# Kernel optimization log

Measured on AMD Instinct MI355X. Metric: run time of the kernel, lower is better.

## Reference

```python
import jax, jax.numpy as jnp
import numpy as np

K = 32          # neighbors per point
EPS = 1e-5      # InstanceNorm eps (torch default)
SLOPE = 0.2     # LeakyReLU negative slope


def _knn(x, k):
    # x: [B, N, C]; squared euclidean distances (same ordering as torch.cdist p=2)
    sq = jnp.sum(x * x, axis=-1)                       # [B, N]
    d = sq[:, :, None] + sq[:, None, :] - 2.0 * jnp.einsum('bnc,bmc->bnm', x, x)
    _, idx = jax.lax.top_k(-d, k + 1)                  # smallest distances first
    return idx[:, :, 1:]                               # drop self -> [B, N, k]


def _edge_feat(x, idx):
    # x: [B, N, C], idx: [B, N, k] -> [B, N, k, 2C] = concat(neighbor - center, center)
    nb = jax.vmap(lambda xb, ib: xb[ib])(x, idx)       # [B, N, k, C] gather
    c = jnp.broadcast_to(x[:, :, None, :], nb.shape)
    return jnp.concatenate([nb - c, c], axis=-1)


def _inorm(x, axes):
    # InstanceNorm (no affine): normalize over `axes` with biased variance
    m = jnp.mean(x, axis=axes, keepdims=True)
    v = jnp.mean((x - m) ** 2, axis=axes, keepdims=True)
    return (x - m) * jax.lax.rsqrt(v + EPS)


def _lrelu(x):
    return jnp.where(x >= 0, x, SLOPE * x)


def setup_inputs() -> dict:
    key = jax.random.key(0)
    ks = jax.random.split(key, 11)
    B, N = 2, 2048

    def w(k, shape):
        return jax.random.normal(k, shape, jnp.float32) * 0.05

    return {
        'x': jax.random.normal(ks[0], (B, N, 3), jnp.float32),
        'n': jax.random.normal(ks[1], (B, N, 3), jnp.float32),
        'W0': w(ks[2], (32, 6)),      # Conv2d(6, 32, 1, bias=False)
        'W1': w(ks[3], (64, 64)),     # Conv2d(64, 64, 1)
        'W2': w(ks[4], (128, 128)),   # Conv2d(128, 128, 1)
        'W3': w(ks[5], (256, 256)),   # Conv2d(256, 256, 1)
        'Wh': w(ks[6], (128, 480)),   # Conv1d(sum(hidden)=480, encod_dim=128, 1)
        'fc1_w': w(ks[7], (128, 128)),
        'fc1_b': w(ks[8], (128,)),
        'fc2_w': w(ks[9], (128, 128)),
        'fc2_b': w(ks[10], (128,)),
    }


def reference(x, n, W0, W1, W2, W3, Wh, fc1_w, fc1_b, fc2_w, fc2_b):
    # include_normals=False: n is accepted but unused (matches torch forward).
    feats = []
    h = x  # [B, N, C], C starts at 3
    for W in (W0, W1, W2, W3):
        idx = _knn(h, K)                              # [B, N, K]
        e = _edge_feat(h, idx)                        # [B, N, K, 2C]
        e = jnp.einsum('bnkc,oc->bnko', e, W)         # 1x1 conv
        e = _lrelu(_inorm(e, (1, 2)))                 # InstanceNorm2d over (N, K)
        h = jnp.max(e, axis=2)                        # max over neighbors -> [B, N, O]
        feats.append(h)
    f = jnp.concatenate(feats, axis=-1)               # [B, N, 480]
    f = jnp.einsum('bnc,oc->bno', f, Wh)              # 1x1 conv1d -> [B, N, 128]
    f = _lrelu(_inorm(f, (1,)))                       # InstanceNorm1d over N; dropout is identity (eval)
    g = jnp.max(f, axis=1)                            # adaptive_max_pool1d(1) -> [B, 128]
    g = g @ fc1_w.T + fc1_b
    # torch InstanceNorm1d on a 2D [B, 128] input treats it as unbatched (C, L):
    # normalizes each row over its 128 features.
    g = _lrelu(_inorm(g, (1,)))
    return g @ fc2_w.T + fc2_b                        # [B, 128]
```

## Files before the change

kernel.cpp:

```cpp
#include <hip/hip_runtime.h>
#include <hip/hip_bf16.h>
#include <cstdint>

using bf16 = __hip_bfloat16;

static constexpr int B = 2;
static constexpr int N = 2048;
static constexpr int KNN = 32;
static constexpr int FD = 480;
static constexpr float EPS = 1e-5f;
static constexpr float SLOPE = 0.2f;
static constexpr int REP = 8;

static constexpr size_t N_XF = (size_t)B * N * 3;
static constexpr size_t N_FEATS = (size_t)B * N * FD;
static constexpr size_t N_DIST = (size_t)B * N * N;
static constexpr size_t N_IDX = (size_t)B * N * KNN;
static constexpr size_t N_PROJ = (size_t)B * N * 512;
static constexpr size_t O_XF = 0;
static constexpr size_t O_FEATS = O_XF + N_XF;
static constexpr size_t O_DIST = O_FEATS + N_FEATS;
static constexpr size_t O_IDX = O_DIST + N_DIST;
static constexpr size_t O_PROJ = O_IDX + N_IDX;
static constexpr size_t O_WP0 = O_PROJ + N_PROJ;
static constexpr size_t O_WP1 = O_WP0 + 192;
static constexpr size_t O_WP2 = O_WP1 + 4096;
static constexpr size_t O_WP3 = O_WP2 + 16384;
static constexpr size_t O_WHT = O_WP3 + 65536;
static constexpr size_t O_F1W = O_WHT + 61440;
static constexpr size_t O_F1B = O_F1W + 16384;
static constexpr size_t O_F2W = O_F1B + 128;
static constexpr size_t O_F2B = O_F2W + 16384;
static constexpr size_t O_FLAG = O_F2B + 128;
static constexpr size_t O_CS0 = O_FLAG + 16;
static constexpr size_t O_CS1 = O_CS0 + (size_t)REP * B * 32 * 2;
static constexpr size_t O_CS2 = O_CS1 + (size_t)REP * B * 64 * 2;
static constexpr size_t O_CS3 = O_CS2 + (size_t)REP * B * 128 * 2;
static constexpr size_t O_FSUM = O_CS3 + (size_t)REP * B * 256 * 2;
static constexpr size_t O_FSS = O_FSUM + 256;
static constexpr size_t O_FMAX = O_FSS + 256;
static constexpr size_t O_END = O_FMAX + 256;
static constexpr size_t N_ZERO = O_END - O_CS0;

__device__ __forceinline__ float lrelu(float x) { return x >= 0.f ? x : SLOPE * x; }

__device__ __forceinline__ float load_in(const void* p, int i, int isf32) {
  return isf32 ? ((const float*)p)[i] : __bfloat162float(((const bf16*)p)[i]);
}

__device__ __forceinline__ unsigned key_of(float f) {
  unsigned u = __float_as_uint(f);
  return (u & 0x80000000u) ? ~u : (u | 0x80000000u);
}

static constexpr int PREP_TOTAL =
    (int)(N_XF + 96 + 2048 + 8192 + 32768 + 61440 + 16384 + 128 + 16384 + 128 + N_ZERO);

__global__ __launch_bounds__(256) void prep_kernel(
    const void* __restrict__ x, const void* __restrict__ W0, const void* __restrict__ W1,
    const void* __restrict__ W2, const void* __restrict__ W3, const void* __restrict__ Wh,
    const void* __restrict__ fc1w, const void* __restrict__ fc1b,
    const void* __restrict__ fc2w, const void* __restrict__ fc2b, float* __restrict__ ws) {
  __shared__ float red[256];
  const unsigned short* xr = (const unsigned short*)x;
  float mx = 0.f;
  for (int i = threadIdx.x; i < B * N * 3; i += 256) {
    float v = __uint_as_float(((unsigned)xr[i]) << 16);
    v = fabsf(v);
    if (!(v < 1e30f)) v = 1e30f;
    mx = fmaxf(mx, v);
  }
  red[threadIdx.x] = mx;
  __syncthreads();
  for (int s = 128; s > 0; s >>= 1) {
    if (threadIdx.x < s) red[threadIdx.x] = fmaxf(red[threadIdx.x], red[threadIdx.x + s]);
    __syncthreads();
  }
  int isf = red[0] > 1e3f ? 1 : 0;
  if (blockIdx.x == 0 && threadIdx.x == 0) ((int*)(ws + O_FLAG))[0] = isf;

  int idx = blockIdx.x * 256 + threadIdx.x;
  if (idx < (int)N_XF) { ws[O_XF + idx] = load_in(x, idx, isf); return; }
  idx -= (int)N_XF;
  if (idx < 96) {
    int o = idx / 3, c = idx - o * 3;
    float a = load_in(W0, o * 6 + c, isf);
    float bb = load_in(W0, o * 6 + 3 + c, isf);
    ws[O_WP0 + c * 64 + o] = a;
    ws[O_WP0 + c * 64 + 32 + o] = bb - a;
    return;
  }
  idx -= 96;
  if (idx < 2048) {
    int o = idx >> 5, c = idx & 31;
    float a = load_in(W1, o * 64 + c, isf);
    float bb = load_in(W1, o * 64 + 32 + c, isf);
    ws[O_WP1 + c * 128 + o] = a;
    ws[O_WP1 + c * 128 + 64 + o] = bb - a;
    return;
  }
  idx -= 2048;
  if (idx < 8192) {
    int o = idx >> 6, c = idx & 63;
    float a = load_in(W2, o * 128 + c, isf);
    float bb = load_in(W2, o * 128 + 64 + c, isf);
    ws[O_WP2 + c * 256 + o] = a;
    ws[O_WP2 + c * 256 + 128 + o] = bb - a;
    return;
  }
  idx -= 8192;
  if (idx < 32768) {
    int o = idx >> 7, c = idx & 127;
    float a = load_in(W3, o * 256 + c, isf);
    float bb = load_in(W3, o * 256 + 128 + c, isf);
    ws[O_WP3 + c * 512 + o] = a;
    ws[O_WP3 + c * 512 + 256 + o] = bb - a;
    return;
  }
  idx -= 32768;
  if (idx < 61440) {
    int o = idx / 480, c = idx - o * 480;
    ws[O_WHT + c * 128 + o] = load_in(Wh, idx, isf);
    return;
  }
  idx -= 61440;
  if (idx < 16384) { ws[O_F1W + idx] = load_in(fc1w, idx, isf); return; }
  idx -= 16384;
  if (idx < 128) { ws[O_F1B + idx] = load_in(fc1b, idx, isf); return; }
  idx -= 128;
  if (idx < 16384) { ws[O_F2W + idx] = load_in(fc2w, idx, isf); return; }
  idx -= 16384;
  if (idx < 128) { ws[O_F2B + idx] = load_in(fc2b, idx, isf); return; }
  idx -= 128;
  if (idx < (int)N_ZERO) ws[O_CS0 + idx] = 0.f;
}

template <int C>
__global__ __launch_bounds__(256) void dist_kernel(const float* __restrict__ h, int hstride,
                                                   unsigned* __restrict__ dist) {
  constexpr int CW = 16;
  __shared__ float Ast[CW][68];
  __shared__ float Bst[CW][132];
  __shared__ float sqn[64], sqm[128];
  int b = blockIdx.z;
  int n0 = blockIdx.y * 64, m0 = blockIdx.x * 128;
  int tid = threadIdx.x;
  int tx = tid & 15, ty = tid >> 4;
  float dot[4][8] = {};
  float sqa = 0.f;
  for (int cc = 0; cc < C; cc += CW) {
    if constexpr (C % CW == 0) {
      int r = tid >> 2, cq = (tid & 3) * 4;
      float4 va = *reinterpret_cast<const float4*>(
          &h[(size_t)(b * N + n0 + r) * hstride + cc + cq]);
      Ast[cq + 0][r] = va.x;
      Ast[cq + 1][r] = va.y;
      Ast[cq + 2][r] = va.z;
      Ast[cq + 3][r] = va.w;
#pragma unroll
      for (int k = 0; k < 2; ++k) {
        int i = tid + k * 256;
        int rB = i >> 2, cqB = (i & 3) * 4;
        float4 vb = *reinterpret_cast<const float4*>(
            &h[(size_t)(b * N + m0 + rB) * hstride + cc + cqB]);
        Bst[cqB + 0][rB] = vb.x;
        Bst[cqB + 1][rB] = vb.y;
        Bst[cqB + 2][rB] = vb.z;
        Bst[cqB + 3][rB] = vb.w;
      }
    } else {
      for (int i = tid; i < 64 * CW; i += 256) {
        int c = i & 15, r = i >> 4;
        int gc = cc + c;
        Ast[c][r] = (gc < C) ? h[(size_t)(b * N + n0 + r) * hstride + gc] : 0.f;
      }
      for (int i = tid; i < 128 * CW; i += 256) {
        int c = i & 15, r = i >> 4;
        int gc = cc + c;
        Bst[c][r] = (gc < C) ? h[(size_t)(b * N + m0 + r) * hstride + gc] : 0.f;
      }
    }
    __syncthreads();
    if (tid < 64) {
#pragma unroll
      for (int c = 0; c < CW; ++c) { float v = Ast[c][tid]; sqa += v * v; }
    } else if (tid < 192) {
      int r = tid - 64;
#pragma unroll
      for (int c = 0; c < CW; ++c) { float v = Bst[c][r]; sqa += v * v; }
    }
#pragma unroll
    for (int c = 0; c < CW; ++c) {
      float4 a0 = *reinterpret_cast<const float4*>(&Ast[c][ty * 4]);
      float4 b0 = *reinterpret_cast<const float4*>(&Bst[c][tx * 4]);
      float4 b1 = *reinterpret_cast<const float4*>(&Bst[c][64 + tx * 4]);
      float av[4] = {a0.x, a0.y, a0.z, a0.w};
      float bv[8] = {b0.x, b0.y, b0.z, b0.w, b1.x, b1.y, b1.z, b1.w};
#pragma unroll
      for (int i = 0; i < 4; ++i)
#pragma unroll
        for (int j = 0; j < 8; ++j) dot[i][j] += av[i] * bv[j];
    }
    __syncthreads();
  }
  if (tid < 64) sqn[tid] = sqa;
  else if (tid < 192) sqm[tid - 64] = sqa;
  __syncthreads();
#pragma unroll
  for (int i = 0; i < 4; ++i) {
    int nn = n0 + ty * 4 + i;
    float sn = sqn[ty * 4 + i];
    uint4 w;
    w.x = key_of(sn + sqm[tx * 4 + 0] - 2.f * dot[i][0]);
    w.y = key_of(sn + sqm[tx * 4 + 1] - 2.f * dot[i][1]);
    w.z = key_of(sn + sqm[tx * 4 + 2] - 2.f * dot[i][2]);
    w.w = key_of(sn + sqm[tx * 4 + 3] - 2.f * dot[i][3]);
    *reinterpret_cast<uint4*>(&dist[(size_t)(b * N + nn) * N + m0 + tx * 4]) = w;
    uint4 w2;
    w2.x = key_of(sn + sqm[64 + tx * 4 + 0] - 2.f * dot[i][4]);
    w2.y = key_of(sn + sqm[64 + tx * 4 + 1] - 2.f * dot[i][5]);
    w2.z = key_of(sn + sqm[64 + tx * 4 + 2] - 2.f * dot[i][6]);
    w2.w = key_of(sn + sqm[64 + tx * 4 + 3] - 2.f * dot[i][7]);
    *reinterpret_cast<uint4*>(&dist[(size_t)(b * N + nn) * N + m0 + 64 + tx * 4]) = w2;
  }
}

__device__ __forceinline__ unsigned long long wave_min_u64(unsigned long long v) {
#pragma unroll
  for (int m = 1; m < 64; m <<= 1) {
    unsigned lo = (unsigned)v;
    unsigned hi = (unsigned)(v >> 32);
    unsigned olo = (unsigned)__shfl_xor((int)lo, m, 64);
    unsigned ohi = (unsigned)__shfl_xor((int)hi, m, 64);
    unsigned long long ov = ((unsigned long long)ohi << 32) | olo;
    if (ov < v) v = ov;
  }
  return v;
}

#define ARGMIN32(dk, ld, lj)                                        \
  {                                                                 \
    unsigned kv0 = dk[0], kv1 = dk[8], kv2 = dk[16], kv3 = dk[24];  \
    int j0 = 0, j1 = 8, j2 = 16, j3 = 24;                           \
    _Pragma("unroll")                                               \
    for (int t = 1; t < 8; ++t) {                                   \
      if (dk[t] < kv0) { kv0 = dk[t]; j0 = t; }                     \
      if (dk[8 + t] < kv1) { kv1 = dk[8 + t]; j1 = 8 + t; }         \
      if (dk[16 + t] < kv2) { kv2 = dk[16 + t]; j2 = 16 + t; }      \
      if (dk[24 + t] < kv3) { kv3 = dk[24 + t]; j3 = 24 + t; }      \
    }                                                               \
    if (kv1 < kv0) { kv0 = kv1; j0 = j1; }                          \
    if (kv3 < kv2) { kv2 = kv3; j2 = j3; }                          \
    if (kv2 < kv0) { kv0 = kv2; j0 = j2; }                          \
    ld = kv0; lj = j0;                                              \
  }

__device__ __forceinline__ unsigned bitonic64_u32(unsigned v, int lane) {
#pragma unroll
  for (int k = 2; k <= 64; k <<= 1) {
#pragma unroll
    for (int j = k >> 1; j > 0; j >>= 1) {
      unsigned o = (unsigned)__shfl_xor((int)v, j, 64);
      bool up = (lane & k) == 0;
      bool lower = (lane & j) == 0;
      bool keepmin = (up == lower);
      unsigned mn = v < o ? v : o;
      unsigned mx = v < o ? o : v;
      v = keepmin ? mn : mx;
    }
  }
  return v;
}

__device__ __forceinline__ void bitonic64_u64(unsigned& hi, unsigned& lo, int lane) {
#pragma unroll
  for (int k = 2; k <= 64; k <<= 1) {
#pragma unroll
    for (int j = k >> 1; j > 0; j >>= 1) {
      unsigned ohi = (unsigned)__shfl_xor((int)hi, j, 64);
      unsigned olo = (unsigned)__shfl_xor((int)lo, j, 64);
      bool up = (lane & k) == 0;
      bool lower = (lane & j) == 0;
      bool keepmin = (up == lower);
      bool lt = (hi < ohi) || (hi == ohi && lo < olo);
      bool take_other = keepmin ? !lt : lt;
      if (take_other) { hi = ohi; lo = olo; }
    }
  }
}

template <int C, int NO2>
__global__ __launch_bounds__(256) void selproj_kernel(const unsigned* __restrict__ dist,
                                                      int* __restrict__ idxb,
                                                      const float* __restrict__ h,
                                                      int hstride,
                                                      const float* __restrict__ Wp,
                                                      float* __restrict__ projb) {
  constexpr int NSEL = B * N / 4;
  constexpr int MT = NO2 / 64;
  constexpr int CW = 16;
  __shared__ float As[64][17];
  __shared__ float Bs[64][17];
  if (blockIdx.x < NSEL) {
    int row = blockIdx.x * 4 + (threadIdx.x >> 6);
    int lane = threadIdx.x & 63;
    const unsigned* drow = dist + (size_t)row * N;
    unsigned dk[32];
#pragma unroll
    for (int j = 0; j < 32; ++j) dk[j] = drow[j * 64 + lane];
    unsigned lmin0 = dk[0], lmin1 = dk[1];
#pragma unroll
    for (int j = 2; j < 32; j += 2) {
      lmin0 = lmin0 < dk[j] ? lmin0 : dk[j];
      lmin1 = lmin1 < dk[j + 1] ? lmin1 : dk[j + 1];
    }
    unsigned lmin = lmin0 < lmin1 ? lmin0 : lmin1;
    unsigned srt = bitonic64_u32(lmin, lane);
    unsigned T = (unsigned)__shfl((int)srt, 32, 64);
    unsigned cnt = 0;
#pragma unroll
    for (int j = 0; j < 32; ++j) cnt += (dk[j] <= T) ? 1u : 0u;
    unsigned inc = cnt;
#pragma unroll
    for (int d = 1; d < 64; d <<= 1) {
      unsigned t = (unsigned)__shfl_up((int)inc, d, 64);
      if (lane >= d) inc += t;
    }
    unsigned tot = (unsigned)__shfl((int)inc, 63, 64);
    unsigned off = inc - cnt;
    bool fast = tot <= 64u;
    unsigned* aHi = reinterpret_cast<unsigned*>(&As[0][0]);
    unsigned* aLo = reinterpret_cast<unsigned*>(&Bs[0][0]);
    int wbase = (threadIdx.x >> 6) * 64;
    aHi[wbase + lane] = 0xFFFFFFFFu;
    aLo[wbase + lane] = 0xFFFFFFFFu;
    __syncthreads();
    if (fast) {
      unsigned o = off;
#pragma unroll
      for (int j = 0; j < 32; ++j) {
        if (dk[j] <= T) {
          aHi[wbase + o] = dk[j];
          aLo[wbase + o] = (unsigned)(j * 64 + lane);
          ++o;
        }
      }
    }
    __syncthreads();
    if (fast) {
      unsigned hi = aHi[wbase + lane];
      unsigned lo = aLo[wbase + lane];
      bitonic64_u64(hi, lo, lane);
      if (lane >= 1 && lane <= KNN) idxb[row * KNN + lane - 1] = (int)lo;
    } else {
      unsigned ld;
      int lj;
      ARGMIN32(dk, ld, lj);
      unsigned saved = 0;
      for (int it = 0; it <= KNN; ++it) {
        unsigned long long lkey =
            ((unsigned long long)ld << 32) | (unsigned)(lj * 64 + lane);
        unsigned long long g = wave_min_u64(lkey);
        if (it > 0 && lane == it - 1) saved = (unsigned)(g & 0xFFFFFFFFull);
        if (lkey == g) {
#pragma unroll
          for (int j = 0; j < 32; ++j)
            if (j == lj) dk[j] = 0xFFFFFFFFu;
          ARGMIN32(dk, ld, lj);
        }
      }
      if (lane < KNN) idxb[row * KNN + lane] = (int)saved;
    }
  } else {
    int tile = blockIdx.x - NSEL;
    int m0 = (tile % MT) * 64;
    int n0 = (tile / MT) * 64;
    int tid = threadIdx.x;
    int tx = tid & 15, ty = tid >> 4;
    float dot[4][4] = {};
    for (int cc = 0; cc < C; cc += CW) {
      for (int i = tid; i < 64 * CW; i += 256) {
        int r = i >> 4, c = i & 15;
        int gc = cc + c;
        As[r][c] = (gc < C) ? h[(size_t)(n0 + r) * hstride + gc] : 0.f;
      }
      for (int i = tid; i < 64 * CW; i += 256) {
        int c = i >> 6, m = i & 63;
        int gc = cc + c;
        Bs[m][c] = (gc < C) ? Wp[(size_t)gc * NO2 + m0 + m] : 0.f;
      }
      __syncthreads();
#pragma unroll
      for (int c = 0; c < CW; ++c) {
        float av[4], bv[4];
#pragma unroll
        for (int i = 0; i < 4; ++i) av[i] = As[ty * 4 + i][c];
#pragma unroll
        for (int j = 0; j < 4; ++j) bv[j] = Bs[tx * 4 + j][c];
#pragma unroll
        for (int i = 0; i < 4; ++i)
#pragma unroll
          for (int j = 0; j < 4; ++j) dot[i][j] += av[i] * bv[j];
      }
      __syncthreads();
    }
#pragma unroll
    for (int i = 0; i < 4; ++i) {
      float4 wv4;
      wv4.x = dot[i][0];
      wv4.y = dot[i][1];
      wv4.z = dot[i][2];
      wv4.w = dot[i][3];
      int m = m0 + tx * 4;
      size_t base = ((size_t)(m >> 4) * (B * N) + (size_t)(n0 + ty * 4 + i)) * 16 + (m & 15);
      *reinterpret_cast<float4*>(&projb[base]) = wv4;
    }
  }
}

template <int O, int NP>
__global__ __launch_bounds__(256) void edge_slab_kernel(const float* __restrict__ projs,
                                                        const int* __restrict__ idxb,
                                                        float* __restrict__ cstats,
                                                        float* __restrict__ featdst) {
  __shared__ float slab[2048 * 16];
  __shared__ float redsm[2][4][16];
  int split = blockIdx.x, s = blockIdx.y, b = blockIdx.z;
  int tid = threadIdx.x, w = tid >> 6, lane = tid & 63;
  int kq = lane >> 4, ch = lane & 15;
  {
    const float4* src =
        (const float4*)(projs + ((size_t)s * (B * N) + (size_t)b * N) * 16);
    float4* dst = (float4*)slab;
#pragma unroll
    for (int i = 0; i < 32; ++i) dst[tid + i * 256] = src[tid + i * 256];
  }
  __syncthreads();
  const float* h0s = projs + (size_t)(O / 16 + s) * (B * N) * 16;
  int bn0 = b * N + split * NP;
  constexpr int NPW = NP / 4;
  float sum = 0.f, ssum = 0.f;
  int bn = bn0 + w;
  int4 j0n = *(const int4*)(idxb + (size_t)bn * KNN + kq * 8);
  int4 j1n = *(const int4*)(idxb + (size_t)bn * KNN + kq * 8 + 4);
  float h0n = h0s[(size_t)bn * 16 + ch];
  for (int p = 0; p < NPW; ++p) {
    int4 j0 = j0n, j1 = j1n;
    float h0 = h0n;
    int bncur = bn;
    if (p + 1 < NPW) {
      bn = bn0 + (p + 1) * 4 + w;
      j0n = *(const int4*)(idxb + (size_t)bn * KNN + kq * 8);
      j1n = *(const int4*)(idxb + (size_t)bn * KNN + kq * 8 + 4);
      h0n = h0s[(size_t)bn * 16 + ch];
    }
    float a0 = slab[j0.x * 16 + ch];
    float a1 = slab[j0.y * 16 + ch];
    float a2 = slab[j0.z * 16 + ch];
    float a3 = slab[j0.w * 16 + ch];
    float a4 = slab[j1.x * 16 + ch];
    float a5 = slab[j1.y * 16 + ch];
    float a6 = slab[j1.z * 16 + ch];
    float a7 = slab[j1.w * 16 + ch];
    float e0 = a0 + h0, e1 = a1 + h0, e2 = a2 + h0, e3 = a3 + h0;
    float e4 = a4 + h0, e5 = a5 + h0, e6 = a6 + h0, e7 = a7 + h0;
    sum += e0 + e1 + e2 + e3 + e4 + e5 + e6 + e7;
    ssum += e0 * e0 + e1 * e1 + e2 * e2 + e3 * e3 + e4 * e4 + e5 * e5 + e6 * e6 + e7 * e7;
    float mx = fmaxf(fmaxf(fmaxf(e0, e1), fmaxf(e2, e3)), fmaxf(fmaxf(e4, e5), fmaxf(e6, e7)));
    mx = fmaxf(mx, __shfl_xor(mx, 16, 64));
    mx = fmaxf(mx, __shfl_xor(mx, 32, 64));
    if (kq == 0) featdst[(size_t)bncur * FD + s * 16 + ch] = mx;
  }
  sum += __shfl_xor(sum, 16, 64);
  sum += __shfl_xor(sum, 32, 64);
  ssum += __shfl_xor(ssum, 16, 64);
  ssum += __shfl_xor(ssum, 32, 64);
  if (kq == 0) {
    redsm[0][w][ch] = sum;
    redsm[1][w][ch] = ssum;
  }
  __syncthreads();
  if (tid < 16) {
    float S = 0.f, SS = 0.f;
#pragma unroll
    for (int r = 0; r < 4; ++r) {
      S += redsm[0][r][tid];
      SS += redsm[1][r][tid];
    }
    int rep = split & (REP - 1);
    float* cs = cstats + ((size_t)rep * B + b) * O * 2 + (size_t)(s * 16 + tid) * 2;
    atomicAdd(&cs[0], S);
    atomicAdd(&cs[1], SS);
  }
}

__global__ void finalize_kernel(const float* __restrict__ cstats,
                                float* __restrict__ featdst, int O) {
  int i = blockIdx.x * 256 + threadIdx.x;
  int o = i % O;
  int bn = i / O;
  int b = bn >> 11;
  float s = 0.f, ss = 0.f;
#pragma unroll
  for (int r = 0; r < REP; ++r) {
    s += cstats[(size_t)r * (B * O * 2) + (size_t)(b * O + o) * 2 + 0];
    ss += cstats[(size_t)r * (B * O * 2) + (size_t)(b * O + o) * 2 + 1];
  }
  constexpr float inv = 1.f / ((float)N * KNN);
  float m = s * inv;
  float v = fmaxf(ss * inv - m * m, 0.f);
  float* p = &featdst[(size_t)bn * FD + o];
  float e = (*p - m) * rsqrtf(v + EPS);
  *p = lrelu(e);
}

__global__ __launch_bounds__(256) void fstage_kernel(const float* __restrict__ feats,
                                                     const float* __restrict__ Wht,
                                                     float* __restrict__ fsum,
                                                     float* __restrict__ fss,
                                                     unsigned* __restrict__ fmaxu) {
  int blk = blockIdx.x;
  int b = blk >> 7;
  int n0 = (blk & 127) * 16;
  int tid = threadIdx.x;
  __shared__ float rows[16][FD];
  __shared__ float red[3][2][128];
  for (int i = tid; i < 16 * FD; i += 256) {
    int r = i / FD, c = i - r * FD;
    rows[r][c] = feats[(size_t)(b * N + n0 + r) * FD + c];
  }
  __syncthreads();
  int o = tid & 127, g = tid >> 7;
  float acc[8] = {};
  for (int c = 0; c < FD; c += 4) {
    float w0 = Wht[(c + 0) * 128 + o];
    float w1 = Wht[(c + 1) * 128 + o];
    float w2 = Wht[(c + 2) * 128 + o];
    float w3 = Wht[(c + 3) * 128 + o];
#pragma unroll
    for (int j = 0; j < 8; ++j) {
      float4 r4 = *reinterpret_cast<const float4*>(&rows[g * 8 + j][c]);
      acc[j] += w0 * r4.x + w1 * r4.y + w2 * r4.z + w3 * r4.w;
    }
  }
  float s = 0.f, ss = 0.f, mx = -3.4e38f;
#pragma unroll
  for (int j = 0; j < 8; ++j) {
    float f = acc[j];
    s += f;
    ss += f * f;
    mx = fmaxf(mx, f);
  }
  red[0][g][o] = s;
  red[1][g][o] = ss;
  red[2][g][o] = mx;
  __syncthreads();
  if (g == 0) {
    s += red[0][1][o];
    ss += red[1][1][o];
    mx = fmaxf(mx, red[2][1][o]);
    atomicAdd(&fsum[b * 128 + o], s);
    atomicAdd(&fss[b * 128 + o], ss);
    unsigned u = __float_as_uint(mx);
    u = (u & 0x80000000u) ? ~u : (u | 0x80000000u);
    atomicMax(&fmaxu[b * 128 + o], u);
  }
}

__global__ __launch_bounds__(128) void head_kernel(const float* __restrict__ fsum,
                                                   const float* __restrict__ fss,
                                                   const unsigned* __restrict__ fmaxu,
                                                   const float* __restrict__ fc1w,
                                                   const float* __restrict__ fc1b,
                                                   const float* __restrict__ fc2w,
                                                   const float* __restrict__ fc2b,
                                                   void* __restrict__ out,
                                                   const int* __restrict__ flag) {
  int b = blockIdx.x, o = threadIdx.x;
  __shared__ float gs[128], t1[128], ys[128];
  constexpr float invN = 1.f / N;
  float m = fsum[b * 128 + o] * invN;
  float v = fmaxf(fss[b * 128 + o] * invN - m * m, 0.f);
  unsigned u = fmaxu[b * 128 + o];
  unsigned bits = (u & 0x80000000u) ? (u ^ 0x80000000u) : ~u;
  float fx = __uint_as_float(bits);
  gs[o] = lrelu((fx - m) * rsqrtf(v + EPS));
  __syncthreads();
  float a = fc1b[o];
  for (int c = 0; c < 128; ++c) a += fc1w[o * 128 + c] * gs[c];
  t1[o] = a;
  __syncthreads();
  float mm = 0.f;
  for (int c = 0; c < 128; ++c) mm += t1[c];
  mm *= (1.f / 128);
  float vv = 0.f;
  for (int c = 0; c < 128; ++c) {
    float d = t1[c] - mm;
    vv += d * d;
  }
  vv *= (1.f / 128);
  ys[o] = lrelu((a - mm) * rsqrtf(vv + EPS));
  __syncthreads();
  float r = fc2b[o];
  for (int c = 0; c < 128; ++c) r += fc2w[o * 128 + c] * ys[c];
  if (flag[0])
    ((float*)out)[b * 128 + o] = r;
  else
    ((bf16*)out)[b * 128 + o] = __float2bfloat16(r);
}

template <int C, int O>
static void run_layer(const float* h, int hstride, float* featdst, const float* Wp,
                      float* cstats, unsigned* dist, float* projb, int* idxb,
                      hipStream_t stream) {
  constexpr int NSEL = B * N / 4;
  constexpr int NPROJ = (2 * O / 64) * (B * N / 64);
  dist_kernel<C><<<dim3(N / 128, N / 64, B), 256, 0, stream>>>(h, hstride, dist);
  selproj_kernel<C, 2 * O><<<NSEL + NPROJ, 256, 0, stream>>>(dist, idxb, h, hstride, Wp,
                                                             projb);
  constexpr int NP = (O >= 256) ? 256 : (O == 128 ? 128 : 64);
  edge_slab_kernel<O, NP><<<dim3(N / NP, O / 16, B), 256, 0, stream>>>(projb, idxb, cstats,
                                                                       featdst);
  finalize_kernel<<<B * N * O / 256, 256, 0, stream>>>(cstats, featdst, O);
}

extern "C" void kernel_launch(void* const* d_in, const int* in_sizes, int n_in,
                              void* d_out, int out_size, void* d_ws, size_t ws_size,
                              hipStream_t stream) {
  float* ws = (float*)d_ws;
  float* xf = ws + O_XF;
  float* feats = ws + O_FEATS;
  unsigned* dist = (unsigned*)(ws + O_DIST);
  float* projb = ws + O_PROJ;
  int* idxb = (int*)(ws + O_IDX);
  int* flag = (int*)(ws + O_FLAG);

  prep_kernel<<<(PREP_TOTAL + 255) / 256, 256, 0, stream>>>(
      d_in[0], d_in[2], d_in[3], d_in[4], d_in[5], d_in[6], d_in[7], d_in[8], d_in[9],
      d_in[10], ws);

  run_layer<3, 32>(xf, 3, feats + 0, ws + O_WP0, ws + O_CS0, dist, projb, idxb, stream);
  run_layer<32, 64>(feats + 0, FD, feats + 32, ws + O_WP1, ws + O_CS1, dist, projb, idxb,
                    stream);
  run_layer<64, 128>(feats + 32, FD, feats + 96, ws + O_WP2, ws + O_CS2, dist, projb, idxb,
                     stream);
  run_layer<128, 256>(feats + 96, FD, feats + 224, ws + O_WP3, ws + O_CS3, dist, projb,
                      idxb, stream);

  fstage_kernel<<<B * 128, 256, 0, stream>>>(feats, ws + O_WHT, ws + O_FSUM, ws + O_FSS,
                                             (unsigned*)(ws + O_FMAX));
  head_kernel<<<B, 128, 0, stream>>>(ws + O_FSUM, ws + O_FSS, (unsigned*)(ws + O_FMAX),
                                     ws + O_F1W, ws + O_F1B, ws + O_F2W, ws + O_F2B, d_out,
                                     flag);
}
```

Baseline: 387.3 us.

## Exploit distance-matrix symmetry by computing only upper-triangle tiles

The pairwise distance kernel now launches only the upper-triangular 64x64 tiles and writes each off-diagonal tile both directly and transposed, roughly halving the dot-product work. Tiles shrink from 64x128 to 64x64, so each block computes a 4x4 register tile per thread. The transposed stores have a strided row pattern (uint4 per row), which may reduce write coalescing. Total dist write traffic stays the same, and the tile index is decoded with a small serial loop.

```diff
diff --git a/kernel.cpp b/kernel.cpp
--- a/kernel.cpp
+++ b/kernel.cpp
@@ -140,13 +140,17 @@
                                                    unsigned* __restrict__ dist) {
   constexpr int CW = 16;
   __shared__ float Ast[CW][68];
-  __shared__ float Bst[CW][132];
-  __shared__ float sqn[64], sqm[128];
-  int b = blockIdx.z;
-  int n0 = blockIdx.y * 64, m0 = blockIdx.x * 128;
+  __shared__ float Bst[CW][68];
+  __shared__ float sqn[64], sqm[64];
+  int b = blockIdx.y;
+  int t = blockIdx.x;
+  int ti = 0;
+  while (t >= 32 - ti) { t -= 32 - ti; ++ti; }
+  int tj = ti + t;
+  int n0 = ti * 64, m0 = tj * 64;
   int tid = threadIdx.x;
   int tx = tid & 15, ty = tid >> 4;
-  float dot[4][8] = {};
+  float dot[4][4] = {};
   float sqa = 0.f;
   for (int cc = 0; cc < C; cc += CW) {
     if constexpr (C % CW == 0) {
@@ -157,26 +161,17 @@
       Ast[cq + 1][r] = va.y;
       Ast[cq + 2][r] = va.z;
       Ast[cq + 3][r] = va.w;
-#pragma unroll
-      for (int k = 0; k < 2; ++k) {
-        int i = tid + k * 256;
-        int rB = i >> 2, cqB = (i & 3) * 4;
-        float4 vb = *reinterpret_cast<const float4*>(
-            &h[(size_t)(b * N + m0 + rB) * hstride + cc + cqB]);
-        Bst[cqB + 0][rB] = vb.x;
-        Bst[cqB + 1][rB] = vb.y;
-        Bst[cqB + 2][rB] = vb.z;
-        Bst[cqB + 3][rB] = vb.w;
-      }
+      float4 vb = *reinterpret_cast<const float4*>(
+          &h[(size_t)(b * N + m0 + r) * hstride + cc + cq]);
+      Bst[cq + 0][r] = vb.x;
+      Bst[cq + 1][r] = vb.y;
+      Bst[cq + 2][r] = vb.z;
+      Bst[cq + 3][r] = vb.w;
     } else {
       for (int i = tid; i < 64 * CW; i += 256) {
         int c = i & 15, r = i >> 4;
         int gc = cc + c;
         Ast[c][r] = (gc < C) ? h[(size_t)(b * N + n0 + r) * hstride + gc] : 0.f;
-      }
-      for (int i = tid; i < 128 * CW; i += 256) {
-        int c = i & 15, r = i >> 4;
-        int gc = cc + c;
         Bst[c][r] = (gc < C) ? h[(size_t)(b * N + m0 + r) * hstride + gc] : 0.f;
       }
     }
@@ -184,7 +179,7 @@
     if (tid < 64) {
 #pragma unroll
       for (int c = 0; c < CW; ++c) { float v = Ast[c][tid]; sqa += v * v; }
-    } else if (tid < 192) {
+    } else if (tid < 128) {
       int r = tid - 64;
 #pragma unroll
       for (int c = 0; c < CW; ++c) { float v = Bst[c][r]; sqa += v * v; }
@@ -193,35 +188,46 @@
     for (int c = 0; c < CW; ++c) {
       float4 a0 = *reinterpret_cast<const float4*>(&Ast[c][ty * 4]);
       float4 b0 = *reinterpret_cast<const float4*>(&Bst[c][tx * 4]);
-      float4 b1 = *reinterpret_cast<const float4*>(&Bst[c][64 + tx * 4]);
       float av[4] = {a0.x, a0.y, a0.z, a0.w};
-      float bv[8] = {b0.x, b0.y, b0.z, b0.w, b1.x, b1.y, b1.z, b1.w};
+      float bv[4] = {b0.x, b0.y, b0.z, b0.w};
 #pragma unroll
       for (int i = 0; i < 4; ++i)
 #pragma unroll
-        for (int j = 0; j < 8; ++j) dot[i][j] += av[i] * bv[j];
+        for (int j = 0; j < 4; ++j) dot[i][j] += av[i] * bv[j];
     }
     __syncthreads();
   }
   if (tid < 64) sqn[tid] = sqa;
-  else if (tid < 192) sqm[tid - 64] = sqa;
-  __syncthreads();
+  else if (tid < 128) sqm[tid - 64] = sqa;
+  __syncthreads();
+  float sm[4];
+#pragma unroll
+  for (int j = 0; j < 4; ++j) sm[j] = sqm[tx * 4 + j];
 #pragma unroll
   for (int i = 0; i < 4; ++i) {
     int nn = n0 + ty * 4 + i;
     float sn = sqn[ty * 4 + i];
     uint4 w;
-    w.x = key_of(sn + sqm[tx * 4 + 0] - 2.f * dot[i][0]);
-    w.y = key_of(sn + sqm[tx * 4 + 1] - 2.f * dot[i][1]);
-    w.z = key_of(sn + sqm[tx * 4 + 2] - 2.f * dot[i][2]);
-    w.w = key_of(sn + sqm[tx * 4 + 3] - 2.f * dot[i][3]);
+    w.x = key_of(sn + sm[0] - 2.f * dot[i][0]);
+    w.y = key_of(sn + sm[1] - 2.f * dot[i][1]);
+    w.z = key_of(sn + sm[2] - 2.f * dot[i][2]);
+    w.w = key_of(sn + sm[3] - 2.f * dot[i][3]);
     *reinterpret_cast<uint4*>(&dist[(size_t)(b * N + nn) * N + m0 + tx * 4]) = w;
-    uint4 w2;
-    w2.x = key_of(sn + sqm[64 + tx * 4 + 0] - 2.f * dot[i][4]);
-    w2.y = key_of(sn + sqm[64 + tx * 4 + 1] - 2.f * dot[i][5]);
-    w2.z = key_of(sn + sqm[64 + tx * 4 + 2] - 2.f * dot[i][6]);
-    w2.w = key_of(sn + sqm[64 + tx * 4 + 3] - 2.f * dot[i][7]);
-    *reinterpret_cast<uint4*>(&dist[(size_t)(b * N + nn) * N + m0 + 64 + tx * 4]) = w2;
+  }
+  if (ti != tj) {
+    float sn4[4];
+#pragma unroll
+    for (int i = 0; i < 4; ++i) sn4[i] = sqn[ty * 4 + i];
+#pragma unroll
+    for (int j = 0; j < 4; ++j) {
+      int mm = m0 + tx * 4 + j;
+      uint4 w;
+      w.x = key_of(sm[j] + sn4[0] - 2.f * dot[0][j]);
+      w.y = key_of(sm[j] + sn4[1] - 2.f * dot[1][j]);
+      w.z = key_of(sm[j] + sn4[2] - 2.f * dot[2][j]);
+      w.w = key_of(sm[j] + sn4[3] - 2.f * dot[3][j]);
+      *reinterpret_cast<uint4*>(&dist[(size_t)(b * N + mm) * N + n0 + ty * 4]) = w;
+    }
   }
 }
 
@@ -615,7 +621,8 @@
                       hipStream_t stream) {
   constexpr int NSEL = B * N / 4;
   constexpr int NPROJ = (2 * O / 64) * (B * N / 64);
-  dist_kernel<C><<<dim3(N / 128, N / 64, B), 256, 0, stream>>>(h, hstride, dist);
+  constexpr int NTRI = 32 * 33 / 2;
+  dist_kernel<C><<<dim3(NTRI, B), 256, 0, stream>>>(h, hstride, dist);
   selproj_kernel<C, 2 * O><<<NSEL + NPROJ, 256, 0, stream>>>(dist, idxb, h, hstride, Wp,
                                                              projb);
   constexpr int NP = (O >= 256) ? 256 : (O == 128 ? 128 : 64);
```

Result: slower. 408.4 us (+5.4%).

## Fuse InstanceNorm+LeakyReLU finalize into consumer kernels' load paths

Applied to the files above, without the earlier changes.

Removes the per-layer finalize kernel that rewrote the pre-norm max features in place. Consumers of each layer's output (the next layer's distance and projection kernels, and the final fstage kernel) now fold the per-channel stats into shared-memory mean/rstd tables and apply normalization plus LeakyReLU as they load. This drops four launches and a read-modify-write pass over the feature buffer. In exchange, normalization is recomputed redundantly in every consumer tile, and stats are folded per block.

```diff
diff --git a/kernel.cpp b/kernel.cpp
--- a/kernel.cpp
+++ b/kernel.cpp
@@ -53,6 +53,20 @@
   return (u & 0x80000000u) ? ~u : (u | 0x80000000u);
 }
 
+__device__ __forceinline__ void fold_stats(const float* __restrict__ cs, int O, int b,
+                                           int c, float& m, float& r) {
+  float s = 0.f, ss = 0.f;
+#pragma unroll
+  for (int rep = 0; rep < REP; ++rep) {
+    s += cs[(size_t)rep * (B * O * 2) + (size_t)(b * O + c) * 2 + 0];
+    ss += cs[(size_t)rep * (B * O * 2) + (size_t)(b * O + c) * 2 + 1];
+  }
+  constexpr float inv = 1.f / ((float)N * KNN);
+  m = s * inv;
+  float v = fmaxf(ss * inv - m * m, 0.f);
+  r = rsqrtf(v + EPS);
+}
+
 static constexpr int PREP_TOTAL =
     (int)(N_XF + 96 + 2048 + 8192 + 32768 + 61440 + 16384 + 128 + 16384 + 128 + N_ZERO);
 
@@ -135,17 +149,27 @@
   if (idx < (int)N_ZERO) ws[O_CS0 + idx] = 0.f;
 }
 
-template <int C>
+template <int C, bool NORM>
 __global__ __launch_bounds__(256) void dist_kernel(const float* __restrict__ h, int hstride,
-                                                   unsigned* __restrict__ dist) {
+                                                   unsigned* __restrict__ dist,
+                                                   const float* __restrict__ csp) {
   constexpr int CW = 16;
   __shared__ float Ast[CW][68];
   __shared__ float Bst[CW][132];
   __shared__ float sqn[64], sqm[128];
+  __shared__ float mtab[128], rtab[128];
   int b = blockIdx.z;
   int n0 = blockIdx.y * 64, m0 = blockIdx.x * 128;
   int tid = threadIdx.x;
   int tx = tid & 15, ty = tid >> 4;
+  if constexpr (NORM) {
+    for (int c = tid; c < C; c += 256) fold_stats(csp, C, b, c, mtab[c], rtab[c]);
+    __syncthreads();
+  }
+  auto nrm = [&](float v, int gc) {
+    if constexpr (NORM) return lrelu((v - mtab[gc]) * rtab[gc]);
+    else return v;
+  };
   float dot[4][8] = {};
   float sqa = 0.f;
   for (int cc = 0; cc < C; cc += CW) {
@@ -153,31 +177,31 @@
       int r = tid >> 2, cq = (tid & 3) * 4;
       float4 va = *reinterpret_cast<const float4*>(
           &h[(size_t)(b * N + n0 + r) * hstride + cc + cq]);
-      Ast[cq + 0][r] = va.x;
-      Ast[cq + 1][r] = va.y;
-      Ast[cq + 2][r] = va.z;
-      Ast[cq + 3][r] = va.w;
+      Ast[cq + 0][r] = nrm(va.x, cc + cq + 0);
+      Ast[cq + 1][r] = nrm(va.y, cc + cq + 1);
+      Ast[cq + 2][r] = nrm(va.z, cc + cq + 2);
+      Ast[cq + 3][r] = nrm(va.w, cc + cq + 3);
 #pragma unroll
       for (int k = 0; k < 2; ++k) {
         int i = tid + k * 256;
         int rB = i >> 2, cqB = (i & 3) * 4;
         float4 vb = *reinterpret_cast<const float4*>(
             &h[(size_t)(b * N + m0 + rB) * hstride + cc + cqB]);
-        Bst[cqB + 0][rB] = vb.x;
-        Bst[cqB + 1][rB] = vb.y;
-        Bst[cqB + 2][rB] = vb.z;
-        Bst[cqB + 3][rB] = vb.w;
+        Bst[cqB + 0][rB] = nrm(vb.x, cc + cqB + 0);
+        Bst[cqB + 1][rB] = nrm(vb.y, cc + cqB + 1);
+        Bst[cqB + 2][rB] = nrm(vb.z, cc + cqB + 2);
+        Bst[cqB + 3][rB] = nrm(vb.w, cc + cqB + 3);
       }
     } else {
       for (int i = tid; i < 64 * CW; i += 256) {
         int c = i & 15, r = i >> 4;
         int gc = cc + c;
-        Ast[c][r] = (gc < C) ? h[(size_t)(b * N + n0 + r) * hstride + gc] : 0.f;
+        Ast[c][r] = (gc < C) ? nrm(h[(size_t)(b * N + n0 + r) * hstride + gc], gc) : 0.f;
       }
       for (int i = tid; i < 128 * CW; i += 256) {
         int c = i & 15, r = i >> 4;
         int gc = cc + c;
-        Bst[c][r] = (gc < C) ? h[(size_t)(b * N + m0 + r) * hstride + gc] : 0.f;
+        Bst[c][r] = (gc < C) ? nrm(h[(size_t)(b * N + m0 + r) * hstride + gc], gc) : 0.f;
       }
     }
     __syncthreads();
@@ -289,18 +313,20 @@
   }
 }
 
-template <int C, int NO2>
+template <int C, int NO2, bool NORM>
 __global__ __launch_bounds__(256) void selproj_kernel(const unsigned* __restrict__ dist,
                                                       int* __restrict__ idxb,
                                                       const float* __restrict__ h,
                                                       int hstride,
                                                       const float* __restrict__ Wp,
-                                                      float* __restrict__ projb) {
+                                                      float* __restrict__ projb,
+                                                      const float* __restrict__ csp) {
   constexpr int NSEL = B * N / 4;
   constexpr int MT = NO2 / 64;
   constexpr int CW = 16;
   __shared__ float As[64][17];
   __shared__ float Bs[64][17];
+  __shared__ float mtab[128], rtab[128];
   if (blockIdx.x < NSEL) {
     int row = blockIdx.x * 4 + (threadIdx.x >> 6);
     int lane = threadIdx.x & 63;
@@ -377,12 +403,22 @@
     int n0 = (tile / MT) * 64;
     int tid = threadIdx.x;
     int tx = tid & 15, ty = tid >> 4;
+    if constexpr (NORM) {
+      int bb = n0 >> 11;
+      for (int c = tid; c < C; c += 256) fold_stats(csp, C, bb, c, mtab[c], rtab[c]);
+      __syncthreads();
+    }
     float dot[4][4] = {};
     for (int cc = 0; cc < C; cc += CW) {
       for (int i = tid; i < 64 * CW; i += 256) {
         int r = i >> 4, c = i & 15;
         int gc = cc + c;
-        As[r][c] = (gc < C) ? h[(size_t)(n0 + r) * hstride + gc] : 0.f;
+        float v = 0.f;
+        if (gc < C) {
+          v = h[(size_t)(n0 + r) * hstride + gc];
+          if constexpr (NORM) v = lrelu((v - mtab[gc]) * rtab[gc]);
+        }
+        As[r][c] = v;
       }
       for (int i = tid; i < 64 * CW; i += 256) {
         int c = i >> 6, m = i & 63;
@@ -494,40 +530,36 @@
   }
 }
 
-__global__ void finalize_kernel(const float* __restrict__ cstats,
-                                float* __restrict__ featdst, int O) {
-  int i = blockIdx.x * 256 + threadIdx.x;
-  int o = i % O;
-  int bn = i / O;
-  int b = bn >> 11;
-  float s = 0.f, ss = 0.f;
-#pragma unroll
-  for (int r = 0; r < REP; ++r) {
-    s += cstats[(size_t)r * (B * O * 2) + (size_t)(b * O + o) * 2 + 0];
-    ss += cstats[(size_t)r * (B * O * 2) + (size_t)(b * O + o) * 2 + 1];
-  }
-  constexpr float inv = 1.f / ((float)N * KNN);
-  float m = s * inv;
-  float v = fmaxf(ss * inv - m * m, 0.f);
-  float* p = &featdst[(size_t)bn * FD + o];
-  float e = (*p - m) * rsqrtf(v + EPS);
-  *p = lrelu(e);
-}
-
 __global__ __launch_bounds__(256) void fstage_kernel(const float* __restrict__ feats,
                                                      const float* __restrict__ Wht,
                                                      float* __restrict__ fsum,
                                                      float* __restrict__ fss,
-                                                     unsigned* __restrict__ fmaxu) {
+                                                     unsigned* __restrict__ fmaxu,
+                                                     const float* __restrict__ cs0,
+                                                     const float* __restrict__ cs1,
+                                                     const float* __restrict__ cs2,
+                                                     const float* __restrict__ cs3) {
   int blk = blockIdx.x;
   int b = blk >> 7;
   int n0 = (blk & 127) * 16;
   int tid = threadIdx.x;
   __shared__ float rows[16][FD];
   __shared__ float red[3][2][128];
+  __shared__ float mtab[FD], rtab[FD];
+  for (int c = tid; c < FD; c += 256) {
+    const float* cs;
+    int O, oc;
+    if (c < 32) { cs = cs0; O = 32; oc = c; }
+    else if (c < 96) { cs = cs1; O = 64; oc = c - 32; }
+    else if (c < 224) { cs = cs2; O = 128; oc = c - 96; }
+    else { cs = cs3; O = 256; oc = c - 224; }
+    fold_stats(cs, O, b, oc, mtab[c], rtab[c]);
+  }
+  __syncthreads();
   for (int i = tid; i < 16 * FD; i += 256) {
     int r = i / FD, c = i - r * FD;
-    rows[r][c] = feats[(size_t)(b * N + n0 + r) * FD + c];
+    float v = feats[(size_t)(b * N + n0 + r) * FD + c];
+    rows[r][c] = lrelu((v - mtab[c]) * rtab[c]);
   }
   __syncthreads();
   int o = tid & 127, g = tid >> 7;
@@ -609,19 +641,19 @@
     ((bf16*)out)[b * 128 + o] = __float2bfloat16(r);
 }
 
-template <int C, int O>
+template <int C, int O, bool NORM>
 static void run_layer(const float* h, int hstride, float* featdst, const float* Wp,
-                      float* cstats, unsigned* dist, float* projb, int* idxb,
-                      hipStream_t stream) {
+                      const float* csprev, float* cstats, unsigned* dist, float* projb,
+                      int* idxb, hipStream_t stream) {
   constexpr int NSEL = B * N / 4;
   constexpr int NPROJ = (2 * O / 64) * (B * N / 64);
-  dist_kernel<C><<<dim3(N / 128, N / 64, B), 256, 0, stream>>>(h, hstride, dist);
-  selproj_kernel<C, 2 * O><<<NSEL + NPROJ, 256, 0, stream>>>(dist, idxb, h, hstride, Wp,
-                                                             projb);
+  dist_kernel<C, NORM><<<dim3(N / 128, N / 64, B), 256, 0, stream>>>(h, hstride, dist,
+                                                                     csprev);
+  selproj_kernel<C, 2 * O, NORM><<<NSEL + NPROJ, 256, 0, stream>>>(dist, idxb, h, hstride,
+                                                                   Wp, projb, csprev);
   constexpr int NP = (O >= 256) ? 256 : (O == 128 ? 128 : 64);
   edge_slab_kernel<O, NP><<<dim3(N / NP, O / 16, B), 256, 0, stream>>>(projb, idxb, cstats,
                                                                        featdst);
-  finalize_kernel<<<B * N * O / 256, 256, 0, stream>>>(cstats, featdst, O);
 }
 
 extern "C" void kernel_launch(void* const* d_in, const int* in_sizes, int n_in,
@@ -639,16 +671,18 @@
       d_in[0], d_in[2], d_in[3], d_in[4], d_in[5], d_in[6], d_in[7], d_in[8], d_in[9],
       d_in[10], ws);
 
-  run_layer<3, 32>(xf, 3, feats + 0, ws + O_WP0, ws + O_CS0, dist, projb, idxb, stream);
-  run_layer<32, 64>(feats + 0, FD, feats + 32, ws + O_WP1, ws + O_CS1, dist, projb, idxb,
-                    stream);
-  run_layer<64, 128>(feats + 32, FD, feats + 96, ws + O_WP2, ws + O_CS2, dist, projb, idxb,
-                     stream);
-  run_layer<128, 256>(feats + 96, FD, feats + 224, ws + O_WP3, ws + O_CS3, dist, projb,
-                      idxb, stream);
+  run_layer<3, 32, false>(xf, 3, feats + 0, ws + O_WP0, nullptr, ws + O_CS0, dist, projb,
+                          idxb, stream);
+  run_layer<32, 64, true>(feats + 0, FD, feats + 32, ws + O_WP1, ws + O_CS0, ws + O_CS1,
+                          dist, projb, idxb, stream);
+  run_layer<64, 128, true>(feats + 32, FD, feats + 96, ws + O_WP2, ws + O_CS1, ws + O_CS2,
+                           dist, projb, idxb, stream);
+  run_layer<128, 256, true>(feats + 96, FD, feats + 224, ws + O_WP3, ws + O_CS2,
+                            ws + O_CS3, dist, projb, idxb, stream);
 
   fstage_kernel<<<B * 128, 256, 0, stream>>>(feats, ws + O_WHT, ws + O_FSUM, ws + O_FSS,
-                                             (unsigned*)(ws + O_FMAX));
+                                             (unsigned*)(ws + O_FMAX), ws + O_CS0,
+                                             ws + O_CS1, ws + O_CS2, ws + O_CS3);
   head_kernel<<<B, 128, 0, stream>>>(ws + O_FSUM, ws + O_FSS, (unsigned*)(ws + O_FMAX),
                                      ws + O_F1W, ws + O_F1B, ws + O_F2W, ws + O_F2B, d_out,
                                      flag);
```

After: 394.8 us. About the same (+1.9%).
